# Performance work log

Measured on AMD Instinct MI355X. Metric: run time of the kernel, lower is better.

Reference implementation:

```python
import jax, jax.numpy as jnp
import numpy as np

B, S, D, H = 4, 1024, 1024, 16
HD = D // H  # head dim 64
EPS = 1e-12

def setup_inputs() -> dict:
    key = jax.random.key(0)
    ks = jax.random.split(key, 10)
    sc = 1.0 / np.sqrt(D)
    return {
        "eeg": jax.random.normal(ks[0], (B, S, D), jnp.float32),
        "pic": jax.random.normal(ks[1], (B, S, D), jnp.float32),
        "Wk": jax.random.normal(ks[2], (D, D), jnp.float32) * sc,
        "bk": jnp.zeros((D,), jnp.float32),
        "Wq": jax.random.normal(ks[3], (D, D), jnp.float32) * sc,
        "bq": jnp.zeros((D,), jnp.float32),
        "Wv": jax.random.normal(ks[4], (D, D), jnp.float32) * sc,
        "bv": jnp.zeros((D,), jnp.float32),
        "Wd": jax.random.normal(ks[5], (D, D), jnp.float32) * sc,
        "bd": jnp.zeros((D,), jnp.float32),
        "ln_w": jnp.ones((D,), jnp.float32),
        "ln_b": jnp.zeros((D,), jnp.float32),
    }

def _heads(x):  # [B,S,D] -> [B,H,S,HD]
    return x.reshape(B, S, H, HD).transpose(0, 2, 1, 3)

def reference(eeg, pic, Wk, bk, Wq, bq, Wv, bv, Wd, bd, ln_w, ln_b):
    k = _heads(eeg @ Wk + bk)
    q = _heads(pic @ Wq + bq)
    v = _heads(pic @ Wv + bv)
    scores = jnp.einsum('bhqd,bhkd->bhqk', q, k) / jnp.sqrt(jnp.float32(HD))
    probs = jax.nn.softmax(scores, axis=-1)  # dropout = identity (eval mode)
    ctx = jnp.einsum('bhqk,bhkd->bhqd', probs, v)
    ctx = ctx.transpose(0, 2, 1, 3).reshape(B, S, D)
    h = ctx @ Wd + bd  # out_dropout = identity (eval)
    x = h + pic
    u = x.mean(-1, keepdims=True)
    s = ((x - u) ** 2).mean(-1, keepdims=True)
    x = (x - u) / jnp.sqrt(s + EPS)
    return ln_w * x + ln_b
```

## Files before the change

kernel.cpp:

```cpp
#include <hip/hip_runtime.h>
#include <hip/hip_bf16.h>

#define BB 4
#define SS 1024
#define DD 1024
#define HH 16
#define HD 64
#define MM (BB * SS)
#define LN_EPS 1e-12f

typedef unsigned short u16;
typedef __attribute__((ext_vector_type(8))) short bf16x8;
typedef __attribute__((ext_vector_type(4))) float f32x4;
typedef __attribute__((ext_vector_type(4))) unsigned short u16x4;
typedef __attribute__((ext_vector_type(8))) unsigned short u16x8;

__device__ __forceinline__ u16 f2bf(float f) {
    __hip_bfloat16 h = __float2bfloat16(f);
    u16 r; __builtin_memcpy(&r, &h, 2); return r;
}
__device__ __forceinline__ float bf2f(u16 u) {
    unsigned v = ((unsigned)u) << 16;
    float f; __builtin_memcpy(&f, &v, 4); return f;
}

typedef const __attribute__((address_space(1))) unsigned int* gas1_t;
typedef __attribute__((address_space(3))) unsigned int* las3_t;
__device__ __forceinline__ void gload16(const void* g, void* s) {
    __builtin_amdgcn_global_load_lds((gas1_t)g, (las3_t)s, 16, 0, 0);
}

__global__ __launch_bounds__(256) void conv2_bf16(
    const float* __restrict__ a, const float* __restrict__ c,
    u16* __restrict__ oa, u16* __restrict__ oc)
{
    const float* in = blockIdx.y ? c : a;
    u16* out = blockIdx.y ? oc : oa;
    size_t i = ((size_t)blockIdx.x * 256 + threadIdx.x) * 8;
    float4 x = *(const float4*)(in + i);
    float4 y = *(const float4*)(in + i + 4);
    u16x8 o;
    o[0]=f2bf(x.x); o[1]=f2bf(x.y); o[2]=f2bf(x.z); o[3]=f2bf(x.w);
    o[4]=f2bf(y.x); o[5]=f2bf(y.y); o[6]=f2bf(y.z); o[7]=f2bf(y.w);
    *(u16x8*)(out + i) = o;
}

__global__ __launch_bounds__(256) void transpose_w4(
    const float* __restrict__ W0, const float* __restrict__ W1,
    const float* __restrict__ W2, const float* __restrict__ W3,
    u16* __restrict__ T0, u16* __restrict__ T1,
    u16* __restrict__ T2, u16* __restrict__ T3)
{
    const int z = blockIdx.z;
    const float* W = (z==0)?W0:(z==1)?W1:(z==2)?W2:W3;
    u16* Wt = (z==0)?T0:(z==1)?T1:(z==2)?T2:T3;

    __shared__ float Ls[64][65];
    const int t = threadIdx.x;
    const int k0 = blockIdx.x * 64, n0 = blockIdx.y * 64;
    #pragma unroll
    for (int i = 0; i < 4; ++i) {
        int r = (t >> 4) + i * 16, c = (t & 15) * 4;
        float4 v = *(const float4*)&W[(size_t)(k0 + r) * DD + n0 + c];
        Ls[r][c] = v.x; Ls[r][c+1] = v.y; Ls[r][c+2] = v.z; Ls[r][c+3] = v.w;
    }
    __syncthreads();
    #pragma unroll
    for (int i = 0; i < 2; ++i) {
        int n = (t >> 3) + i * 32, kc = (t & 7) * 8;
        u16x8 o;
        #pragma unroll
        for (int j = 0; j < 8; ++j) o[j] = f2bf(Ls[kc + j][n]);
        *(u16x8*)&Wt[(size_t)(n0 + n) * DD + k0 + kc] = o;
    }
}

template<int TRANS>
__device__ __forceinline__ void gemm128_loop(
    const u16* __restrict__ A, const u16* __restrict__ Bt,
    int bm, int bn, u16* As, u16* Bs, f32x4 (&acc)[4][4])
{
    const int tid = threadIdx.x;
    const int w = tid >> 6, l = tid & 63, g = l >> 4, lr = l & 15;
    const int wm = w >> 1, wn = w & 1;

    for (int k0 = 0; k0 < DD; k0 += 64) {
        #pragma unroll
        for (int rr = 0; rr < 4; ++rr) {
            int Cc = rr * 256 + tid;
            int row = Cc >> 3, s2 = Cc & 7, gc = s2 ^ (row & 7);
            gload16(A + (size_t)(bm + row) * DD + k0 + gc * 8,
                    As + (rr * 256 + w * 64) * 8);
        }
        #pragma unroll
        for (int rr = 0; rr < 4; ++rr) {
            int Cc = rr * 256 + tid;
            int row = Cc >> 3, s2 = Cc & 7, gc = s2 ^ (row & 7);
            gload16(Bt + (size_t)(bn + row) * DD + k0 + gc * 8,
                    Bs + (rr * 256 + w * 64) * 8);
        }
        __syncthreads();

        #pragma unroll
        for (int kh = 0; kh < 2; ++kh) {
            bf16x8 af[4], bfr[4];
            #pragma unroll
            for (int mi = 0; mi < 4; ++mi) {
                int row = wm * 64 + mi * 16 + lr;
                af[mi] = *(const bf16x8*)((const char*)As + row * 128 +
                                          ((kh * 4 + g) ^ (row & 7)) * 16);
            }
            #pragma unroll
            for (int ni = 0; ni < 4; ++ni) {
                int row = wn * 64 + ni * 16 + lr;
                bfr[ni] = *(const bf16x8*)((const char*)Bs + row * 128 +
                                           ((kh * 4 + g) ^ (row & 7)) * 16);
            }
            #pragma unroll
            for (int mi = 0; mi < 4; ++mi)
                #pragma unroll
                for (int ni = 0; ni < 4; ++ni) {
                    if (TRANS)
                        acc[ni][mi] = __builtin_amdgcn_mfma_f32_16x16x32_bf16(
                            bfr[ni], af[mi], acc[ni][mi], 0, 0, 0);
                    else
                        acc[mi][ni] = __builtin_amdgcn_mfma_f32_16x16x32_bf16(
                            af[mi], bfr[ni], acc[mi][ni], 0, 0, 0);
                }
        }
        __syncthreads();
    }
}

__global__ __launch_bounds__(256) void gemm_qkv(
    const u16* __restrict__ Ae, const u16* __restrict__ Ap,
    const u16* __restrict__ Bk, const u16* __restrict__ Bq, const u16* __restrict__ Bv,
    const float* __restrict__ bk, const float* __restrict__ bq, const float* __restrict__ bv,
    u16* __restrict__ Kb, u16* __restrict__ Qb, u16* __restrict__ VtG)
{
    const int sel = blockIdx.y;
    int x = (int)blockIdx.x;
    int sw = (x & 7) * 32 + (x >> 3);
    const int bm = (sw & 31) * 128;
    const int bn = (sw >> 5) * 128;

    const u16* A  = sel ? Ap : Ae;
    const u16* Bt = (sel == 0) ? Bk : (sel == 1) ? Bq : Bv;
    const float* bias = (sel == 0) ? bk : (sel == 1) ? bq : bv;
    const float alpha = (sel == 1) ? 0.180336880111120f : 1.0f;

    __shared__ __align__(16) u16 As[128 * 64];
    __shared__ __align__(16) u16 Bs[128 * 64];

    f32x4 acc[4][4];
    #pragma unroll
    for (int i = 0; i < 4; ++i)
        #pragma unroll
        for (int j = 0; j < 4; ++j) { f32x4 z = {0,0,0,0}; acc[i][j] = z; }

    const int tid = threadIdx.x;
    const int w = tid >> 6, l = tid & 63, g = l >> 4, lr = l & 15;
    const int wm = w >> 1, wn = w & 1;

    if (sel == 2) {
        gemm128_loop<1>(A, Bt, bm, bn, As, Bs, acc);
        #pragma unroll
        for (int ni = 0; ni < 4; ++ni)
            #pragma unroll
            for (int r = 0; r < 4; ++r) {
                int n = bn + wn * 64 + ni * 16 + g * 4 + r;
                float bb = bias[n];
                #pragma unroll
                for (int mi = 0; mi < 4; ++mi) {
                    int m = bm + wm * 64 + mi * 16 + lr;
                    VtG[(size_t)n * MM + m] = f2bf(acc[ni][mi][r] + bb);
                }
            }
    } else {
        gemm128_loop<0>(A, Bt, bm, bn, As, Bs, acc);
        u16* C = sel ? Qb : Kb;
        float b4[4];
        #pragma unroll
        for (int ni = 0; ni < 4; ++ni) b4[ni] = bias[bn + wn * 64 + ni * 16 + lr];
        #pragma unroll
        for (int mi = 0; mi < 4; ++mi)
            #pragma unroll
            for (int ni = 0; ni < 4; ++ni)
                #pragma unroll
                for (int r = 0; r < 4; ++r) {
                    int row = bm + wm * 64 + mi * 16 + g * 4 + r;
                    int col = bn + wn * 64 + ni * 16 + lr;
                    C[(size_t)row * DD + col] = f2bf(alpha * (acc[mi][ni][r] + b4[ni]));
                }
    }
}

__global__ __launch_bounds__(256) void gemm_plain(
    const u16* __restrict__ A, const u16* __restrict__ Bt,
    const float* __restrict__ bias, u16* __restrict__ C)
{
    int x = (int)blockIdx.x;
    int sw = (x & 7) * 32 + (x >> 3);
    const int bm = (sw & 31) * 128;
    const int bn = (sw >> 5) * 128;

    __shared__ __align__(16) u16 As[128 * 64];
    __shared__ __align__(16) u16 Bs[128 * 64];

    f32x4 acc[4][4];
    #pragma unroll
    for (int i = 0; i < 4; ++i)
        #pragma unroll
        for (int j = 0; j < 4; ++j) { f32x4 z = {0,0,0,0}; acc[i][j] = z; }

    gemm128_loop<0>(A, Bt, bm, bn, As, Bs, acc);

    const int tid = threadIdx.x;
    const int w = tid >> 6, l = tid & 63, g = l >> 4, lr = l & 15;
    const int wm = w >> 1, wn = w & 1;
    float b4[4];
    #pragma unroll
    for (int ni = 0; ni < 4; ++ni) b4[ni] = bias[bn + wn * 64 + ni * 16 + lr];
    #pragma unroll
    for (int mi = 0; mi < 4; ++mi)
        #pragma unroll
        for (int ni = 0; ni < 4; ++ni)
            #pragma unroll
            for (int r = 0; r < 4; ++r) {
                int row = bm + wm * 64 + mi * 16 + g * 4 + r;
                int col = bn + wn * 64 + ni * 16 + lr;
                C[(size_t)row * DD + col] = f2bf(acc[mi][ni][r] + b4[ni]);
            }
}

__global__ __launch_bounds__(512) void attn_mfma(
    const u16* __restrict__ Q, const u16* __restrict__ K,
    const u16* __restrict__ Vt, u16* __restrict__ O)
{
    const int tid = threadIdx.x;
    const int w = tid >> 6, l = tid & 63, g = l >> 4, lr = l & 15;
    int bid = (int)blockIdx.x;
    bid = (bid & 7) * 64 + (bid >> 3);
    const int qb = bid & 7, h = (bid >> 3) & 15, b = bid >> 7;
    const size_t qrow0 = (size_t)b * SS + qb * 128;
    const size_t kv0 = (size_t)b * SS;
    const int hc = h * HD;

    __shared__ __align__(16) u16 Ks[2][64 * 64];
    __shared__ __align__(16) u16 Vs[2][64 * 64];
    __shared__ __align__(16) u16 Ps[8][16 * 72];

    const int srow = tid >> 3, ss = tid & 7;
    const int sgc = ss ^ (srow & 7);
    const u16* kg = K + (kv0 + srow) * DD + hc + sgc * 8;
    const u16* vg = Vt + (size_t)(hc + srow) * MM + kv0 + sgc * 8;

    bf16x8 qf[2];
    {
        const u16* qp = Q + (qrow0 + w * 16 + lr) * DD + hc + g * 8;
        qf[0] = *(const bf16x8*)(qp);
        qf[1] = *(const bf16x8*)(qp + 32);
    }

    f32x4 acc[4];
    #pragma unroll
    for (int dt = 0; dt < 4; ++dt) { f32x4 z = {0,0,0,0}; acc[dt] = z; }
    float m_run = -1e30f, l_run = 0.f;

    gload16(kg, &Ks[0][w * 512]);
    gload16(vg, &Vs[0][w * 512]);
    __syncthreads();

    for (int kb = 0; kb < SS / 64; ++kb) {
        const int cur = kb & 1;
        if (kb < SS / 64 - 1) {
            gload16(kg + (size_t)(kb + 1) * 64 * DD, &Ks[cur ^ 1][w * 512]);
            gload16(vg + (size_t)(kb + 1) * 64, &Vs[cur ^ 1][w * 512]);
        }
        const char* kbase = (const char*)&Ks[cur][0];
        const char* vbase = (const char*)&Vs[cur][0];

        f32x4 st[4];
        __builtin_amdgcn_s_setprio(1);
        #pragma unroll
        for (int kt = 0; kt < 4; ++kt) {
            int row = kt * 16 + lr;
            const char* rb = kbase + row * 128;
            bf16x8 k0 = *(const bf16x8*)(rb + ((0 + g) ^ (row & 7)) * 16);
            bf16x8 k1 = *(const bf16x8*)(rb + ((4 + g) ^ (row & 7)) * 16);
            f32x4 z = {0,0,0,0};
            z = __builtin_amdgcn_mfma_f32_16x16x32_bf16(k0, qf[0], z, 0, 0, 0);
            z = __builtin_amdgcn_mfma_f32_16x16x32_bf16(k1, qf[1], z, 0, 0, 0);
            st[kt] = z;
        }
        __builtin_amdgcn_s_setprio(0);

        float tmax = -1e30f;
        #pragma unroll
        for (int kt = 0; kt < 4; ++kt)
            #pragma unroll
            for (int r = 0; r < 4; ++r) tmax = fmaxf(tmax, st[kt][r]);
        tmax = fmaxf(tmax, __shfl_xor(tmax, 16));
        tmax = fmaxf(tmax, __shfl_xor(tmax, 32));

        if (!__all(tmax <= m_run + 8.f)) {
            float m_new = fmaxf(m_run, tmax);
            float sc = exp2f(m_run - m_new);
            m_run = m_new;
            l_run *= sc;
            float scq[4];
            #pragma unroll
            for (int r = 0; r < 4; ++r) scq[r] = __shfl(sc, g * 4 + r);
            #pragma unroll
            for (int dt = 0; dt < 4; ++dt)
                #pragma unroll
                for (int r = 0; r < 4; ++r) acc[dt][r] *= scq[r];
        }

        float p[16];
        float ps = 0.f;
        #pragma unroll
        for (int kt = 0; kt < 4; ++kt)
            #pragma unroll
            for (int r = 0; r < 4; ++r) {
                float v = exp2f(st[kt][r] - m_run);
                p[kt * 4 + r] = v;
                ps += v;
            }
        ps += __shfl_xor(ps, 16);
        ps += __shfl_xor(ps, 32);
        l_run += ps;

        #pragma unroll
        for (int kt = 0; kt < 4; ++kt) {
            u16x4 h4;
            #pragma unroll
            for (int r = 0; r < 4; ++r) h4[r] = f2bf(p[kt * 4 + r]);
            *(u16x4*)((char*)&Ps[w][0] + lr * 144 + kt * 32 + g * 8) = h4;
        }

        __builtin_amdgcn_s_setprio(1);
        #pragma unroll
        for (int kh = 0; kh < 2; ++kh) {
            bf16x8 pf = *(const bf16x8*)((const char*)&Ps[w][0] + lr * 144 +
                                         kh * 64 + g * 16);
            #pragma unroll
            for (int dt = 0; dt < 4; ++dt) {
                int row = dt * 16 + lr;
                bf16x8 vf = *(const bf16x8*)(vbase + row * 128 +
                                             ((kh * 4 + g) ^ (row & 7)) * 16);
                acc[dt] = __builtin_amdgcn_mfma_f32_16x16x32_bf16(pf, vf, acc[dt], 0, 0, 0);
            }
        }
        __builtin_amdgcn_s_setprio(0);

        __syncthreads();
    }

    float invl[4];
    #pragma unroll
    for (int r = 0; r < 4; ++r) invl[r] = 1.f / __shfl(l_run, g * 4 + r);
    #pragma unroll
    for (int dt = 0; dt < 4; ++dt)
        #pragma unroll
        for (int r = 0; r < 4; ++r) {
            size_t row = qrow0 + w * 16 + g * 4 + r;
            O[row * DD + hc + dt * 16 + lr] = f2bf(acc[dt][r] * invl[r]);
        }
}

__global__ __launch_bounds__(256) void ln_kernel(
    const u16* __restrict__ Hs, const float* __restrict__ P,
    const float* __restrict__ w, const float* __restrict__ bshift,
    float* __restrict__ out)
{
    const int row = blockIdx.x;
    const int tid = threadIdx.x;
    const size_t off = (size_t)row * DD;
    const int c0 = tid * 4;

    u16x4 h4 = *(const u16x4*)&Hs[off + c0];
    float4 p4 = *(const float4*)&P[off + c0];
    float x[4];
    x[0] = bf2f(h4[0]) + p4.x; x[1] = bf2f(h4[1]) + p4.y;
    x[2] = bf2f(h4[2]) + p4.z; x[3] = bf2f(h4[3]) + p4.w;

    float s = x[0] + x[1] + x[2] + x[3];
    #pragma unroll
    for (int o = 32; o >= 1; o >>= 1) s += __shfl_xor(s, o, 64);

    __shared__ float r1[4], r2[4];
    const int wid = tid >> 6;
    if ((tid & 63) == 0) r1[wid] = s;
    __syncthreads();
    const float mean = (r1[0] + r1[1] + r1[2] + r1[3]) * (1.f / (float)DD);

    float d2 = 0.f;
    #pragma unroll
    for (int i = 0; i < 4; ++i) { float d = x[i] - mean; d2 += d * d; }
    #pragma unroll
    for (int o = 32; o >= 1; o >>= 1) d2 += __shfl_xor(d2, o, 64);
    if ((tid & 63) == 0) r2[wid] = d2;
    __syncthreads();
    const float var = (r2[0] + r2[1] + r2[2] + r2[3]) * (1.f / (float)DD);
    const float inv = rsqrtf(var + LN_EPS);

    float4 o4;
    o4.x = w[c0 + 0] * ((x[0] - mean) * inv) + bshift[c0 + 0];
    o4.y = w[c0 + 1] * ((x[1] - mean) * inv) + bshift[c0 + 1];
    o4.z = w[c0 + 2] * ((x[2] - mean) * inv) + bshift[c0 + 2];
    o4.w = w[c0 + 3] * ((x[3] - mean) * inv) + bshift[c0 + 3];
    *(float4*)&out[off + c0] = o4;
}

extern "C" void kernel_launch(void* const* d_in, const int* in_sizes, int n_in,
                              void* d_out, int out_size, void* d_ws, size_t ws_size,
                              hipStream_t stream)
{
    const float* eeg = (const float*)d_in[0];
    const float* pic = (const float*)d_in[1];
    const float* Wk  = (const float*)d_in[2];
    const float* bk  = (const float*)d_in[3];
    const float* Wq  = (const float*)d_in[4];
    const float* bq  = (const float*)d_in[5];
    const float* Wv  = (const float*)d_in[6];
    const float* bv  = (const float*)d_in[7];
    const float* Wd  = (const float*)d_in[8];
    const float* bd  = (const float*)d_in[9];
    const float* lnw = (const float*)d_in[10];
    const float* lnb = (const float*)d_in[11];
    float* out = (float*)d_out;

    u16* ws = (u16*)d_ws;
    const size_t M4 = (size_t)1 << 22;
    u16* Ae  = ws;
    u16* Ap  = ws + M4;
    u16* WtK = ws + 2 * M4;
    u16* WtQ = WtK + (1u << 20);
    u16* WtV = WtQ + (1u << 20);
    u16* WtD = WtV + (1u << 20);
    u16* Kb  = ws + 3 * M4;
    u16* Qb  = ws + 4 * M4;
    u16* VtG = ws + 5 * M4;
    u16* Cb  = ws + 6 * M4;
    u16* Hb  = ws + 7 * M4;

    conv2_bf16<<<dim3(2048, 2), 256, 0, stream>>>(eeg, pic, Ae, Ap);
    transpose_w4<<<dim3(16, 16, 4), 256, 0, stream>>>(Wk, Wq, Wv, Wd,
                                                      WtK, WtQ, WtV, WtD);

    gemm_qkv<<<dim3(256, 3), 256, 0, stream>>>(Ae, Ap, WtK, WtQ, WtV,
                                               bk, bq, bv, Kb, Qb, VtG);

    attn_mfma<<<BB * HH * (SS / 128), 512, 0, stream>>>(Qb, Kb, VtG, Cb);

    gemm_plain<<<256, 256, 0, stream>>>(Cb, WtD, bd, Hb);

    ln_kernel<<<MM, 256, 0, stream>>>(Hb, pic, lnw, lnb, out);
}
```

Baseline: 129.7 us.

## Double-buffer GEMM LDS tiles and remap blocks for XCD-aware L2 locality

The GEMM main loop now uses two LDS buffers, issuing the next k-tile's global-to-LDS loads before computing on the current tile, with one barrier per iteration instead of two. Per-thread global pointers are precomputed once. The block-index mapping is also reworked so consecutive blocks on the same XCD (i&7) share B-column tiles and neighbouring A rows, and the QKV launch is flattened to 1D. This doubles LDS use per block (64KB), which may reduce occupancy.

```diff
diff --git a/kernel.cpp b/kernel.cpp
--- a/kernel.cpp
+++ b/kernel.cpp
@@ -75,6 +75,17 @@
     }
 }
 
+__device__ __forceinline__ void stage_tile(
+    const u16* Ag, const u16* Bg, int k0, u16* Asb, u16* Bsb, int w)
+{
+    #pragma unroll
+    for (int rr = 0; rr < 4; ++rr)
+        gload16(Ag + (size_t)rr * 32 * DD + k0, Asb + (rr * 256 + w * 64) * 8);
+    #pragma unroll
+    for (int rr = 0; rr < 4; ++rr)
+        gload16(Bg + (size_t)rr * 32 * DD + k0, Bsb + (rr * 256 + w * 64) * 8);
+}
+
 template<int TRANS>
 __device__ __forceinline__ void gemm128_loop(
     const u16* __restrict__ A, const u16* __restrict__ Bt,
@@ -84,36 +95,35 @@
     const int w = tid >> 6, l = tid & 63, g = l >> 4, lr = l & 15;
     const int wm = w >> 1, wn = w & 1;
 
-    for (int k0 = 0; k0 < DD; k0 += 64) {
-        #pragma unroll
-        for (int rr = 0; rr < 4; ++rr) {
-            int Cc = rr * 256 + tid;
-            int row = Cc >> 3, s2 = Cc & 7, gc = s2 ^ (row & 7);
-            gload16(A + (size_t)(bm + row) * DD + k0 + gc * 8,
-                    As + (rr * 256 + w * 64) * 8);
-        }
-        #pragma unroll
-        for (int rr = 0; rr < 4; ++rr) {
-            int Cc = rr * 256 + tid;
-            int row = Cc >> 3, s2 = Cc & 7, gc = s2 ^ (row & 7);
-            gload16(Bt + (size_t)(bn + row) * DD + k0 + gc * 8,
-                    Bs + (rr * 256 + w * 64) * 8);
-        }
-        __syncthreads();
-
+    const int srow = tid >> 3, ss = tid & 7;
+    const int sgc = ss ^ (srow & 7);
+    const u16* Ag = A + (size_t)(bm + srow) * DD + sgc * 8;
+    const u16* Bg = Bt + (size_t)(bn + srow) * DD + sgc * 8;
+
+    stage_tile(Ag, Bg, 0, As, Bs, w);
+    __syncthreads();
+
+    for (int t = 0; t < 16; ++t) {
+        const int cur = t & 1;
+        if (t < 15)
+            stage_tile(Ag, Bg, (t + 1) * 64,
+                       As + (cur ^ 1) * 8192, Bs + (cur ^ 1) * 8192, w);
+
+        const char* Ab = (const char*)(As + cur * 8192);
+        const char* Bb = (const char*)(Bs + cur * 8192);
         #pragma unroll
         for (int kh = 0; kh < 2; ++kh) {
             bf16x8 af[4], bfr[4];
             #pragma unroll
             for (int mi = 0; mi < 4; ++mi) {
                 int row = wm * 64 + mi * 16 + lr;
-                af[mi] = *(const bf16x8*)((const char*)As + row * 128 +
+                af[mi] = *(const bf16x8*)(Ab + row * 128 +
                                           ((kh * 4 + g) ^ (row & 7)) * 16);
             }
             #pragma unroll
             for (int ni = 0; ni < 4; ++ni) {
                 int row = wn * 64 + ni * 16 + lr;
-                bfr[ni] = *(const bf16x8*)((const char*)Bs + row * 128 +
+                bfr[ni] = *(const bf16x8*)(Bb + row * 128 +
                                            ((kh * 4 + g) ^ (row & 7)) * 16);
             }
             #pragma unroll
@@ -138,25 +148,25 @@
     const float* __restrict__ bk, const float* __restrict__ bq, const float* __restrict__ bv,
     u16* __restrict__ Kb, u16* __restrict__ Qb, u16* __restrict__ VtG)
 {
-    const int sel = blockIdx.y;
-    int x = (int)blockIdx.x;
-    int sw = (x & 7) * 32 + (x >> 3);
-    const int bm = (sw & 31) * 128;
-    const int bn = (sw >> 5) * 128;
+    const int i = (int)blockIdx.x;
+    const int x = i & 7, j = i >> 3;
+    const int sel = j >> 5;
+    const int bn = ((j & 31) >> 2) * 128;
+    const int bm = (x * 4 + (j & 3)) * 128;
 
     const u16* A  = sel ? Ap : Ae;
     const u16* Bt = (sel == 0) ? Bk : (sel == 1) ? Bq : Bv;
     const float* bias = (sel == 0) ? bk : (sel == 1) ? bq : bv;
     const float alpha = (sel == 1) ? 0.180336880111120f : 1.0f;
 
-    __shared__ __align__(16) u16 As[128 * 64];
-    __shared__ __align__(16) u16 Bs[128 * 64];
+    __shared__ __align__(16) u16 As[2 * 128 * 64];
+    __shared__ __align__(16) u16 Bs[2 * 128 * 64];
 
     f32x4 acc[4][4];
     #pragma unroll
-    for (int i = 0; i < 4; ++i)
-        #pragma unroll
-        for (int j = 0; j < 4; ++j) { f32x4 z = {0,0,0,0}; acc[i][j] = z; }
+    for (int a = 0; a < 4; ++a)
+        #pragma unroll
+        for (int b = 0; b < 4; ++b) { f32x4 z = {0,0,0,0}; acc[a][b] = z; }
 
     const int tid = threadIdx.x;
     const int w = tid >> 6, l = tid & 63, g = l >> 4, lr = l & 15;
@@ -199,19 +209,19 @@
     const u16* __restrict__ A, const u16* __restrict__ Bt,
     const float* __restrict__ bias, u16* __restrict__ C)
 {
-    int x = (int)blockIdx.x;
-    int sw = (x & 7) * 32 + (x >> 3);
-    const int bm = (sw & 31) * 128;
-    const int bn = (sw >> 5) * 128;
-
-    __shared__ __align__(16) u16 As[128 * 64];
-    __shared__ __align__(16) u16 Bs[128 * 64];
+    const int i = (int)blockIdx.x;
+    const int x = i & 7, j = i >> 3;
+    const int bn = (j >> 2) * 128;
+    const int bm = (x * 4 + (j & 3)) * 128;
+
+    __shared__ __align__(16) u16 As[2 * 128 * 64];
+    __shared__ __align__(16) u16 Bs[2 * 128 * 64];
 
     f32x4 acc[4][4];
     #pragma unroll
-    for (int i = 0; i < 4; ++i)
-        #pragma unroll
-        for (int j = 0; j < 4; ++j) { f32x4 z = {0,0,0,0}; acc[i][j] = z; }
+    for (int a = 0; a < 4; ++a)
+        #pragma unroll
+        for (int b = 0; b < 4; ++b) { f32x4 z = {0,0,0,0}; acc[a][b] = z; }
 
     gemm128_loop<0>(A, Bt, bm, bn, As, Bs, acc);
 
@@ -449,8 +459,8 @@
     transpose_w4<<<dim3(16, 16, 4), 256, 0, stream>>>(Wk, Wq, Wv, Wd,
                                                       WtK, WtQ, WtV, WtD);
 
-    gemm_qkv<<<dim3(256, 3), 256, 0, stream>>>(Ae, Ap, WtK, WtQ, WtV,
-                                               bk, bq, bv, Kb, Qb, VtG);
+    gemm_qkv<<<768, 256, 0, stream>>>(Ae, Ap, WtK, WtQ, WtV,
+                                      bk, bq, bv, Kb, Qb, VtG);
 
     attn_mfma<<<BB * HH * (SS / 128), 512, 0, stream>>>(Qb, Kb, VtG, Cb);
 
```

New measurement: 136.8 us. +5.5%, slower.
